# Optimization experiments

Hardware: AMD Instinct MI355X
Metric: run time of the kernel (lower is better)

Reference implementation:

```python
import jax, jax.numpy as jnp
from jax import lax
import numpy as np

COMMITMENT_COST = 0.25
N_EMBED = 512
EDIM = 32


def _conv(x, w, b, stride, pad):
    # x: NCHW, w: OIHW (torch Conv2d layout)
    y = lax.conv_general_dilated(x, w, (stride, stride), [(pad, pad), (pad, pad)],
                                 dimension_numbers=("NCHW", "OIHW", "NCHW"))
    return y + b[None, :, None, None]


def _conv_t(x, w, b, stride, pad):
    # torch ConvTranspose2d weight layout: (in, out, kH, kW)
    k = w.shape[2]
    w_ = jnp.flip(w, (2, 3)).transpose(1, 0, 2, 3)  # -> OIHW
    p = k - 1 - pad
    y = lax.conv_general_dilated(x, w_, (1, 1), [(p, p), (p, p)],
                                 lhs_dilation=(stride, stride),
                                 dimension_numbers=("NCHW", "OIHW", "NCHW"))
    return y + b[None, :, None, None]


def setup_inputs() -> dict:
    key = jax.random.key(0)
    ks = jax.random.split(key, 9)
    rn = lambda k, s: jax.random.normal(k, s, jnp.float32) * 0.05
    return {
        "x": jax.random.normal(ks[0], (32, 3, 256, 256), jnp.float32),
        "e_w1": rn(ks[1], (64, 3, 4, 4)),    "e_b1": jnp.zeros((64,), jnp.float32),
        "e_w2": rn(ks[2], (128, 64, 4, 4)),  "e_b2": jnp.zeros((128,), jnp.float32),
        "e_w3": rn(ks[3], (32, 128, 3, 3)),  "e_b3": jnp.zeros((32,), jnp.float32),
        "embed": jax.random.uniform(ks[4], (N_EMBED, EDIM), jnp.float32,
                                    -1.0 / N_EMBED, 1.0 / N_EMBED),
        "d_w1": rn(ks[5], (32, 128, 3, 3)),  "d_b1": jnp.zeros((128,), jnp.float32),
        "d_w2": rn(ks[6], (128, 64, 4, 4)),  "d_b2": jnp.zeros((64,), jnp.float32),
        "d_w3": rn(ks[7], (64, 3, 4, 4)),    "d_b3": jnp.zeros((3,), jnp.float32),
    }


def reference(x, e_w1, e_b1, e_w2, e_b2, e_w3, e_b3, embed,
              d_w1, d_b1, d_w2, d_b2, d_w3, d_b3):
    # ---- encoder ----
    h = jax.nn.relu(_conv(x, e_w1, e_b1, 2, 1))   # [B,64,128,128]
    h = jax.nn.relu(_conv(h, e_w2, e_b2, 2, 1))   # [B,128,64,64]
    z = jax.nn.relu(_conv(h, e_w3, e_b3, 1, 1))   # [B,32,64,64]
    # ---- vector quantizer ----
    zp = z.transpose(0, 2, 3, 1)                  # BHWC
    zf = zp.reshape(-1, EDIM)                     # [N, 32]
    d = (zf ** 2).sum(1, keepdims=True) + (embed ** 2).sum(1) \
        - 2.0 * zf @ embed.T                      # [N, n_embed]
    idx = jnp.argmin(d, axis=1)                   # [N]
    z_q = embed[idx].reshape(zp.shape)            # gather == onehot @ embed
    sg = lax.stop_gradient
    loss = jnp.mean((sg(z_q) - zp) ** 2) + COMMITMENT_COST * jnp.mean((z_q - sg(zp)) ** 2)
    z_q_st = zp + sg(z_q - zp)                    # straight-through
    z_q_st = z_q_st.transpose(0, 3, 1, 2)         # back to NCHW
    # ---- decoder ----
    h = jax.nn.relu(_conv_t(z_q_st, d_w1, d_b1, 1, 1))  # [B,128,64,64]
    h = jax.nn.relu(_conv_t(h, d_w2, d_b2, 2, 1))       # [B,64,128,128]
    x_recon = _conv_t(h, d_w3, d_b3, 2, 1)              # [B,3,256,256]
    return x_recon, loss
```

## Files before the change

### kernel.cpp

```cpp
#include <hip/hip_runtime.h>


typedef __attribute__((ext_vector_type(8))) short     short8;
typedef __attribute__((ext_vector_type(4))) short     s16x4;
typedef __attribute__((ext_vector_type(8))) __bf16    bf16x8;
typedef __attribute__((ext_vector_type(4))) float     f32x4;
typedef __attribute__((ext_vector_type(4))) unsigned  uint32x4;

__device__ __forceinline__ float b2f(unsigned short b) {
  union { unsigned u; float f; } v; v.u = ((unsigned)b) << 16; return v.f;
}
__device__ __forceinline__ unsigned short f2b(float f) {
  union { float f; unsigned u; } v; v.f = f;
  unsigned r = v.u + 0x7FFF + ((v.u >> 16) & 1);
  return (unsigned short)(r >> 16);
}

__global__ __launch_bounds__(256) void prepall_k(
    const float* __restrict__ ew1, const float* __restrict__ ew2,
    const float* __restrict__ ew3, const float* __restrict__ dw1,
    const float* __restrict__ dw2, const float* __restrict__ dw3,
    const float* __restrict__ emb,
    unsigned short* __restrict__ wq1, unsigned short* __restrict__ wq2,
    unsigned short* __restrict__ wq3, unsigned short* __restrict__ wq4,
    unsigned short* __restrict__ wq5, unsigned short* __restrict__ wq6,
    unsigned short* __restrict__ wqe, float* __restrict__ eng) {
  const int b = blockIdx.x;
  if (b < 64) {
    const int i = b*256 + threadIdx.x;
    const int j = i & 7, l = (i >> 3) & 63, ni = (i >> 9) & 3, nc = i >> 11;
    const int lm = l & 15, lk = l >> 4;
    wqe[i] = f2b(emb[(nc*64 + ni*16 + lm)*32 + lk*8 + j]);
    if (i < 512) {
      float s = 0.f;
      #pragma unroll
      for (int k = 0; k < 32; ++k) {
        const float f = b2f(f2b(emb[i*32 + k]));
        s = fmaf(f, f, s);
      }
      eng[i] = s;
    }
  } else if (b < 80) {
    const int i = (b - 64)*256 + threadIdx.x;
    const int j = i & 7, l = (i >> 3) & 63, ni = (i >> 9) & 3, ks = i >> 11;
    const int k = ks*32 + (l >> 4)*8 + j;
    const int co = ni*16 + (l & 15);
    wq1[i] = (k < 48) ? f2b(ew1[co*48 + k]) : (unsigned short)0;
  } else if (b < 592) {
    const int i = (b - 80)*256 + threadIdx.x;
    const int j = i & 7, l = (i >> 3) & 63, ni = (i >> 9) & 7, ks = i >> 12;
    const int lm = l & 15, lk = l >> 4;
    const int tap = ks >> 1, cc = ks & 1;
    const int co = ni*16 + lm, ci = cc*32 + lk*8 + j;
    wq2[i] = f2b(ew2[(co*64 + ci)*16 + tap]);
  } else if (b < 736) {
    const int i = (b - 592)*256 + threadIdx.x;
    const int j = i & 7, l = (i >> 3) & 63, ni = (i >> 9) & 1, ks = i >> 10;
    const int lm = l & 15, lk = l >> 4;
    const int tap = ks >> 2, cf = ks & 3;
    const int co = ni*16 + lm, ci = cf*32 + lk*8 + j;
    wq3[i] = f2b(ew3[(co*128 + ci)*9 + tap]);
  } else if (b < 880) {
    const int i = (b - 736)*256 + threadIdx.x;
    const int j = i & 7, l = (i >> 3) & 63, ni = (i >> 9) & 7, tap = i >> 12;
    const int lm = l & 15, lk = l >> 4;
    const int co = ni*16 + lm, ci = lk*8 + j;
    wq4[i] = f2b(dw1[(ci*128 + co)*9 + (8 - tap)]);
  } else if (b < 1392) {
    const int i = (b - 880)*256 + threadIdx.x;
    const int j = i & 7, l = (i >> 3) & 63, ni = (i >> 9) & 3;
    const int ks = (i >> 11) & 15, p = i >> 15;
    const int lm = l & 15, lk = l >> 4;
    const int py = p >> 1, px = p & 1;
    const int a = ks >> 3, bb = (ks >> 2) & 1, cc = ks & 3;
    const int co = ni*16 + lm, ci = cc*32 + lk*8 + j;
    const int ky = 3 - 2*a - py, kx = 3 - 2*bb - px;
    wq5[i] = f2b(dw2[(ci*64 + co)*16 + ky*4 + kx]);
  } else {
    const int i = (b - 1392)*256 + threadIdx.x;
    const int j = i & 7, l = (i >> 3) & 63, kc = (i >> 9) & 7, p = i >> 12;
    const int lm = l & 15, lk = l >> 4;
    const int a = kc >> 2, bb = (kc >> 1) & 1, ch = kc & 1;
    const int ci = ch*32 + lk*8 + j, co = lm;
    const int py = p >> 1, px = p & 1;
    const int ky = 2 - 2*a + (1 - py), kx = 2 - 2*bb + (1 - px);
    wq6[i] = (co < 3) ? f2b(dw3[(ci*3 + co)*16 + ky*4 + kx]) : (unsigned short)0;
  }
}

__global__ __launch_bounds__(256) void conv1m_k(const float* __restrict__ x,
    const unsigned short* __restrict__ wv, const float* __restrict__ bias,
    unsigned short* __restrict__ out) {
  __shared__ __align__(16) short RAW[12*264];
  __shared__ __align__(16) short IC[128*64];
  const int wid = ((blockIdx.x & 7) << 9) + (blockIdx.x >> 3);
  const int q = wid & 127, n = wid >> 7;
  for (int i = threadIdx.x; i < 396; i += 256)
    *(short8*)&RAW[i*8] = (short8)(short)0;
  __syncthreads();
  for (int s = threadIdx.x; s < 768; s += 256) {
    const int g = s >> 6, seg = s & 63;
    const int ci = g >> 2, ky = g & 3;
    const int iy = 2*q - 1 + ky;
    if (iy >= 0 && iy < 256) {
      const f32x4 v = *(const f32x4*)&x[((n*3 + ci)*256 + iy)*256 + seg*4];
      s16x4 sv;
      #pragma unroll
      for (int e = 0; e < 4; ++e) sv[e] = (short)f2b(v[e]);
      *(s16x4*)&RAW[g*264 + 4 + seg*4] = sv;
    }
  }
  __syncthreads();
  for (int s = threadIdx.x; s < 1024; s += 256) {
    const int kb = s & 7, ox = s >> 3;
    short8 v = (short8)(short)0;
    if (kb < 6) {
      const unsigned* u0 = (const unsigned*)&RAW[(2*kb  )*264 + 2*ox + 2];
      const unsigned* u1 = (const unsigned*)&RAW[(2*kb+1)*264 + 2*ox + 2];
      const unsigned a0 = u0[0], a1 = u0[1], a2 = u0[2];
      const unsigned b0 = u1[0], b1 = u1[1], b2 = u1[2];
      uint32x4 uv;
      uv[0] = (a0 >> 16) | (a1 << 16);
      uv[1] = (a1 >> 16) | (a2 << 16);
      uv[2] = (b0 >> 16) | (b1 << 16);
      uv[3] = (b1 >> 16) | (b2 << 16);
      v = __builtin_bit_cast(short8, uv);
    }
    const int bo = ((ox << 7) + (kb << 4)) ^ ((ox & 7) << 4);
    *(short8*)((char*)IC + bo) = v;
  }
  __syncthreads();
  const int w = threadIdx.x >> 6, l = threadIdx.x & 63;
  const int lm = l & 15, lk = l >> 4;
  f32x4 acc[2][4];
  #pragma unroll
  for (int mi = 0; mi < 2; ++mi)
    #pragma unroll
    for (int ni = 0; ni < 4; ++ni) acc[mi][ni] = (f32x4)0.0f;
  #pragma unroll
  for (int ks = 0; ks < 2; ++ks) {
    short8 bv[4];
    #pragma unroll
    for (int ni = 0; ni < 4; ++ni)
      bv[ni] = *(const short8*)(wv + (((ks*4 + ni)*64 + l) << 3));
    #pragma unroll
    for (int mi = 0; mi < 2; ++mi) {
      const int ox = w*32 + mi*16 + lm;
      const int bo = ((ox << 7) + (ks << 6) + (lk << 4)) ^ ((ox & 7) << 4);
      const short8 av = *(const short8*)((const char*)IC + bo);
      #pragma unroll
      for (int ni = 0; ni < 4; ++ni)
        acc[mi][ni] = __builtin_amdgcn_mfma_f32_16x16x32_bf16(
            __builtin_bit_cast(bf16x8, av),
            __builtin_bit_cast(bf16x8, bv[ni]),
            acc[mi][ni], 0, 0, 0);
    }
  }
  __syncthreads();
  #pragma unroll
  for (int mi = 0; mi < 2; ++mi)
    #pragma unroll
    for (int ni = 0; ni < 4; ++ni) {
      const int co = ni*16 + lm;
      const float bv = bias[co];
      #pragma unroll
      for (int r = 0; r < 4; ++r) {
        const int ox = w*32 + mi*16 + lk*4 + r;
        const int bo = ((ox << 7) + 2*co) ^ ((ox & 7) << 4);
        *(short*)((char*)IC + bo) = (short)f2b(fmaxf(acc[mi][ni][r] + bv, 0.f));
      }
    }
  __syncthreads();
  const long ob = ((long)(n*128 + q)) * 8192;
  for (int s = threadIdx.x; s < 1024; s += 256) {
    const int kb = s & 7, ox = s >> 3;
    const int bo = ((ox << 7) + (kb << 4)) ^ ((ox & 7) << 4);
    *(short8*)&out[ob + ox*64 + kb*8] = *(const short8*)((const char*)IC + bo);
  }
}

#define C2_LOAD(c) \
  _Pragma("unroll") \
  for (int s = 0; s < 9; ++s) { \
    st[s] = (short8)(short)0; \
    if (goff[s] >= 0) st[s] = *(const short8*)(in + goff[s] + (c)*32); \
  }
#define C2_WRITE \
  _Pragma("unroll") \
  for (int s = 0; s < 9; ++s) \
    if (lb[s] >= 0) *(short8*)((char*)IL + lb[s]) = st[s];
#define C2_COMPUTE(c) \
  _Pragma("unroll") \
  for (int t = 0; t < 16; ++t) { \
    const int ky = t >> 2, kx = t & 3; \
    const int p = 1 - (kx & 1), d = kx >> 1; \
    const short8 bv0 = *(const short8*)(wb + (t*2 + (c))*4096); \
    const short8 bv1 = *(const short8*)(wb + (t*2 + (c))*4096 + 512); \
    const char* Ab = (const char*)IL + (Bd0 + d*64); \
    const int imm0 = ((ky*2 + p)*66) << 6; \
    _Pragma("unroll") \
    for (int mi = 0; mi < 4; ++mi) { \
      const short8 av = *(const short8*)(Ab + imm0 + mi*1024); \
      acc[mi][0] = __builtin_amdgcn_mfma_f32_16x16x32_bf16( \
          __builtin_bit_cast(bf16x8, av), __builtin_bit_cast(bf16x8, bv0), \
          acc[mi][0], 0, 0, 0); \
      acc[mi][1] = __builtin_amdgcn_mfma_f32_16x16x32_bf16( \
          __builtin_bit_cast(bf16x8, av), __builtin_bit_cast(bf16x8, bv1), \
          acc[mi][1], 0, 0, 0); \
    } \
  }
__global__ __launch_bounds__(256) void conv2m_k(const unsigned short* __restrict__ in,
    const unsigned short* __restrict__ wv, const float* __restrict__ bias,
    unsigned short* __restrict__ out) {
  __shared__ short IL[8*66*32];
  const int wid = (blockIdx.x & 7)*256 + (blockIdx.x >> 3);
  const int q = wid & 63, n = wid >> 6;
  const int w = threadIdx.x >> 6, l = threadIdx.x & 63;
  const int lm = l & 15, lk = l >> 4;
  const int Bd0 = lm*64 + lk*16;
  const unsigned short* wb = wv + w*1024 + l*8;
  int goff[9], lb[9];
  #pragma unroll
  for (int s = 0; s < 9; ++s) {
    const int i = threadIdx.x + s*256;
    const int part = i & 3, e = i >> 2;
    const int idx = e % 66, rp = e / 66;
    const int r = rp >> 1, p = rp & 1;
    const int iy = 2*q - 1 + r, ix = 2*idx - p;
    const bool ok = (i < 2112) && iy >= 0 && iy < 128 && ix >= 0 && ix < 128;
    goff[s] = ok ? (((n*128 + iy)*128 + ix)*64 + part*8) : -1;
    lb[s]   = (i < 2112) ? (e*64 + part*16) : -1;
  }
  f32x4 acc[4][2];
  #pragma unroll
  for (int mi = 0; mi < 4; ++mi)
    #pragma unroll
    for (int ni = 0; ni < 2; ++ni) acc[mi][ni] = (f32x4)0.0f;
  short8 st[9];
  C2_LOAD(0); C2_WRITE;
  __syncthreads();
  C2_LOAD(1);
  C2_COMPUTE(0);
  __syncthreads();
  C2_WRITE;
  __syncthreads();
  C2_COMPUTE(1);
  __syncthreads();
  short* PB = (short*)IL;
  #pragma unroll
  for (int mi = 0; mi < 4; ++mi)
    #pragma unroll
    for (int r = 0; r < 4; ++r) {
      const int ox = mi*16 + lk*4 + r;
      #pragma unroll
      for (int ni = 0; ni < 2; ++ni) {
        const int co = (w*2 + ni)*16 + lm;
        PB[ox*144 + co] = (short)f2b(fmaxf(acc[mi][ni][r] + bias[co], 0.f));
      }
    }
  __syncthreads();
  {
    const int pos = threadIdx.x >> 2, coq = (threadIdx.x & 3) << 5;
    const long ob = ((long)((n*64 + q)*64 + pos))*128 + coq;
    #pragma unroll
    for (int u2 = 0; u2 < 4; ++u2)
      *(short8*)&out[ob + u2*8] = *(const short8*)&PB[pos*144 + coq + u2*8];
  }
}

#define C3_LOAD(c) \
  _Pragma("unroll") \
  for (int s = 0; s < 9; ++s) { \
    st[s] = (short8)(short)0; \
    if (goff[s] >= 0) st[s] = *(const short8*)(in + goff[s] + (c)*64); \
  }
#define C3_WRITE \
  _Pragma("unroll") \
  for (int s = 0; s < 9; ++s) \
    if (lb[s] >= 0) *(short8*)((char*)IL + lb[s]) = st[s];
#define C3_COMPUTE(c) \
  _Pragma("unroll") \
  for (int u = 0; u < 18; ++u) { \
    const int tap = u >> 1, cc = u & 1; \
    const int ky = tap / 3, kx = tap % 3; \
    const int ks = tap*4 + (c)*2 + cc; \
    const short8 bv0 = *(const short8*)(wb + ks*1024); \
    const short8 bv1 = *(const short8*)(wb + ks*1024 + 512); \
    const char* Ab = (const char*)IL + (Wc[kx][cc]); \
    const int imm0 = ky*8448; \
    _Pragma("unroll") \
    for (int mi = 0; mi < 2; ++mi) { \
      const short8 av = *(const short8*)(Ab + imm0 + mi*2048); \
      acc[mi][0] = __builtin_amdgcn_mfma_f32_16x16x32_bf16( \
          __builtin_bit_cast(bf16x8, av), __builtin_bit_cast(bf16x8, bv0), \
          acc[mi][0], 0, 0, 0); \
      acc[mi][1] = __builtin_amdgcn_mfma_f32_16x16x32_bf16( \
          __builtin_bit_cast(bf16x8, av), __builtin_bit_cast(bf16x8, bv1), \
          acc[mi][1], 0, 0, 0); \
    } \
  }
__global__ __launch_bounds__(256) void conv3v_k(const unsigned short* __restrict__ in,
    const unsigned short* __restrict__ wv, const float* __restrict__ bias,
    const unsigned short* __restrict__ wqe, const float* __restrict__ eng,
    const float* __restrict__ emb, float* __restrict__ zq,
    float* __restrict__ part) {
  __shared__ short IL[4*66*64];
  const int wid = (blockIdx.x & 7)*128 + (blockIdx.x >> 3);
  const int q = wid & 31, n = wid >> 5;
  const int w = threadIdx.x >> 6, l = threadIdx.x & 63;
  const int lm = l & 15, lk = l >> 4;
  const int row = w >> 1, oxb = (w & 1) * 32;
  int goff[9], lb[9];
  #pragma unroll
  for (int s = 0; s < 9; ++s) {
    const int i = threadIdx.x + s*256;
    const int part_ = i & 7, e = i >> 3;
    const int col = e % 66, r = e / 66;
    const int iy = 2*q - 1 + r, ix = col - 1;
    const bool ok = (i < 2112) && iy >= 0 && iy < 64 && ix >= 0 && ix < 64;
    goff[s] = ok ? (((n*64 + iy)*64 + ix)*128 + part_*8) : -1;
    lb[s]   = (i < 2112) ? ((e << 7) + ((part_ << 4) ^ ((col & 7) << 4))) : -1;
  }
  int Wc[3][2];
  #pragma unroll
  for (int kx = 0; kx < 3; ++kx) {
    const int e = oxb + lm + kx;
    Wc[kx][0] = row*8448 + (e << 7) + ((lk << 4) ^ ((e & 7) << 4));
    Wc[kx][1] = Wc[kx][0] ^ 0x40;
  }
  const unsigned short* wb = wv + l*8;
  f32x4 acc[2][2];
  #pragma unroll
  for (int mi = 0; mi < 2; ++mi)
    #pragma unroll
    for (int ni = 0; ni < 2; ++ni) acc[mi][ni] = (f32x4)0.0f;
  short8 st[9];
  C3_LOAD(0); C3_WRITE;
  __syncthreads();
  C3_LOAD(1);
  C3_COMPUTE(0);
  __syncthreads();
  C3_WRITE;
  __syncthreads();
  C3_COMPUTE(1);
  __syncthreads();
  short* ZB  = (short*)IL;
  float* ZF  = (float*)((char*)IL + 10240);
  int*  bidx = (int*)((char*)IL + 28672);
  float* red = (float*)((char*)IL + 29184);
  #pragma unroll
  for (int mi = 0; mi < 2; ++mi)
    #pragma unroll
    for (int ni = 0; ni < 2; ++ni) {
      const int co = ni*16 + lm;
      const float bv = bias[co];
      #pragma unroll
      for (int r = 0; r < 4; ++r) {
        const int pos = row*64 + oxb + mi*16 + lk*4 + r;
        const float v = fmaxf(acc[mi][ni][r] + bv, 0.f);
        ZB[pos*40 + co] = (short)f2b(v);
        ZF[pos*36 + co] = v;
      }
    }
  __syncthreads();
  short8 av[2];
  #pragma unroll
  for (int mi = 0; mi < 2; ++mi)
    av[mi] = *(const short8*)&ZB[(row*64 + oxb + mi*16 + lm)*40 + lk*8];
  float bd[2][4]; int bj[2][4];
  #pragma unroll
  for (int mi = 0; mi < 2; ++mi)
    #pragma unroll
    for (int r = 0; r < 4; ++r) { bd[mi][r] = 1e30f; bj[mi][r] = 0; }
  for (int nc = 0; nc < 8; ++nc) {
    f32x4 a2[2][4];
    #pragma unroll
    for (int mi = 0; mi < 2; ++mi)
      #pragma unroll
      for (int ni = 0; ni < 4; ++ni) a2[mi][ni] = (f32x4)0.0f;
    #pragma unroll
    for (int ni = 0; ni < 4; ++ni) {
      const short8 bv = *(const short8*)(wqe + (((nc*4 + ni)*64 + l) << 3));
      #pragma unroll
      for (int mi = 0; mi < 2; ++mi)
        a2[mi][ni] = __builtin_amdgcn_mfma_f32_16x16x32_bf16(
            __builtin_bit_cast(bf16x8, av[mi]),
            __builtin_bit_cast(bf16x8, bv),
            a2[mi][ni], 0, 0, 0);
    }
    #pragma unroll
    for (int ni = 0; ni < 4; ++ni) {
      const int j = nc*64 + ni*16 + lm;
      const float e_n = eng[j];
      #pragma unroll
      for (int mi = 0; mi < 2; ++mi)
        #pragma unroll
        for (int r = 0; r < 4; ++r) {
          const float d = fmaf(-2.f, a2[mi][ni][r], e_n);
          if (d < bd[mi][r]) { bd[mi][r] = d; bj[mi][r] = j; }
        }
    }
  }
  #pragma unroll
  for (int mi = 0; mi < 2; ++mi)
    #pragma unroll
    for (int r = 0; r < 4; ++r) {
      float d = bd[mi][r]; int j = bj[mi][r];
      #pragma unroll
      for (int off = 1; off < 16; off <<= 1) {
        const float od = __shfl_xor(d, off);
        const int   oj = __shfl_xor(j, off);
        if (od < d || (od == d && oj < j)) { d = od; j = oj; }
      }
      if (lm == 0) bidx[row*64 + oxb + mi*16 + lk*4 + r] = j;
    }
  __syncthreads();
  const int pl = threadIdx.x >> 1, hf = (threadIdx.x & 1) * 16;
  const int code = bidx[pl];
  const int oy2 = 2*q + (pl >> 6), ox2 = pl & 63;
  const long zqo = ((long)((n*64 + oy2)*64 + ox2)) * 32 + hf;
  float se = 0.f;
  #pragma unroll
  for (int qq = 0; qq < 4; ++qq) {
    const f32x4 ev = *(const f32x4*)&emb[code*32 + hf + qq*4];
    const f32x4 zv = *(const f32x4*)&ZF[pl*36 + hf + qq*4];
    *(f32x4*)&zq[zqo + qq*4] = ev;
    const f32x4 df = ev - zv;
    #pragma unroll
    for (int e = 0; e < 4; ++e) se = fmaf(df[e], df[e], se);
  }
  red[threadIdx.x] = se; __syncthreads();
  for (int s2 = 128; s2 > 0; s2 >>= 1) {
    if (threadIdx.x < s2) red[threadIdx.x] += red[threadIdx.x + s2];
    __syncthreads();
  }
  if (threadIdx.x == 0) part[blockIdx.x] = red[0];
}

__global__ __launch_bounds__(256) void d1m_k(const float* __restrict__ in,
    const unsigned short* __restrict__ wv, const float* __restrict__ bias,
    unsigned short* __restrict__ out) {
  __shared__ short IL[264*40];
  const int wid = (blockIdx.x & 7)*128 + (blockIdx.x >> 3);
  const int q = wid & 31, n = wid >> 5;
  const int w = threadIdx.x >> 6, l = threadIdx.x & 63;
  const int lm = l & 15, lk = l >> 4;
  const int row = w >> 1, oxb = (w & 1) * 32;
  for (int i = threadIdx.x; i < 1056; i += 256) {
    const int part = i & 3, e = i >> 2;
    const int col = e % 66, r = e / 66;
    const int iy = 2*q - 1 + r, ix = col - 1;
    short8 v = (short8)(short)0;
    if (iy >= 0 && iy < 64 && ix >= 0 && ix < 64) {
      const float* p = in + (((long)((n*64 + iy)*64 + ix)) * 32 + part*8);
      const f32x4 f0 = *(const f32x4*)p;
      const f32x4 f1 = *(const f32x4*)(p + 4);
      #pragma unroll
      for (int e2 = 0; e2 < 4; ++e2) {
        v[e2]     = (short)f2b(f0[e2]);
        v[e2 + 4] = (short)f2b(f1[e2]);
      }
    }
    *(short8*)&IL[e*40 + part*8] = v;
  }
  const unsigned short* wb = wv + l*8;
  int Wd[3];
  #pragma unroll
  for (int kx = 0; kx < 3; ++kx)
    Wd[kx] = row*5280 + (oxb + lm + kx)*80 + lk*16;
  __syncthreads();
  f32x4 acc[2][8];
  #pragma unroll
  for (int mi = 0; mi < 2; ++mi)
    #pragma unroll
    for (int ni = 0; ni < 8; ++ni) acc[mi][ni] = (f32x4)0.0f;
  #pragma unroll
  for (int tap = 0; tap < 9; ++tap) {
    const int ky = tap / 3, kx = tap % 3;
    short8 bv[8];
    #pragma unroll
    for (int ni = 0; ni < 8; ++ni)
      bv[ni] = *(const short8*)(wb + (tap*8 + ni)*512);
    const char* Ab = (const char*)IL + Wd[kx];
    const int imm0 = ky*5280;
    #pragma unroll
    for (int mi = 0; mi < 2; ++mi) {
      const short8 av = *(const short8*)(Ab + imm0 + mi*1280);
      #pragma unroll
      for (int ni = 0; ni < 8; ++ni)
        acc[mi][ni] = __builtin_amdgcn_mfma_f32_16x16x32_bf16(
            __builtin_bit_cast(bf16x8, av),
            __builtin_bit_cast(bf16x8, bv[ni]),
            acc[mi][ni], 0, 0, 0);
    }
  }
  short* PB = (short*)IL;
  #pragma unroll
  for (int rp = 0; rp < 2; ++rp) {
    __syncthreads();
    if (row == rp) {
      #pragma unroll
      for (int mi = 0; mi < 2; ++mi)
        #pragma unroll
        for (int r = 0; r < 4; ++r) {
          const int ox = oxb + mi*16 + lk*4 + r;
          #pragma unroll
          for (int ni = 0; ni < 8; ++ni) {
            const int co = ni*16 + lm;
            PB[ox*144 + co] = (short)f2b(fmaxf(acc[mi][ni][r] + bias[co], 0.f));
          }
        }
    }
    __syncthreads();
    const int pos = threadIdx.x >> 2, coq = (threadIdx.x & 3) << 5;
    const long ob = ((long)((n*64 + 2*q + rp)*64 + pos))*128 + coq;
    #pragma unroll
    for (int u2 = 0; u2 < 4; ++u2)
      *(short8*)&out[ob + u2*8] = *(const short8*)&PB[pos*144 + coq + u2*8];
  }
}

#define CT2_LOAD(c) \
  _Pragma("unroll") \
  for (int s = 0; s < 7; ++s) { \
    st[s] = (short8)(short)0; \
    if (goff[s] >= 0) st[s] = *(const short8*)(in + goff[s] + (c)*64); \
  }
#define CT2_WRITE \
  _Pragma("unroll") \
  for (int s = 0; s < 7; ++s) \
    if (lb[s] >= 0) *(short8*)((char*)IL + lb[s]) = st[s];
#define CT2_COMPUTE(c) \
  _Pragma("unroll") \
  for (int u = 0; u < 8; ++u) { \
    const int a = u >> 2, b = (u >> 1) & 1, c1 = u & 1; \
    const int ks = (a << 3) | (b << 2) | (2*(c) + c1); \
    short8 bv[4]; \
    _Pragma("unroll") \
    for (int ni = 0; ni < 4; ++ni) \
      bv[ni] = *(const short8*)(wb + ks*2048 + ni*512); \
    const char* Ab = (const char*)IL + (pyb + Wb[b][c1]); \
    const int imm0 = a*8448; \
    _Pragma("unroll") \
    for (int mi = 0; mi < 4; ++mi) { \
      const short8 av = *(const short8*)(Ab + imm0 + mi*2048); \
      _Pragma("unroll") \
      for (int ni = 0; ni < 4; ++ni) \
        acc[mi][ni] = __builtin_amdgcn_mfma_f32_16x16x32_bf16( \
            __builtin_bit_cast(bf16x8, av), \
            __builtin_bit_cast(bf16x8, bv[ni]), \
            acc[mi][ni], 0, 0, 0); \
    } \
  }
__global__ __launch_bounds__(256) void convt2m_k(const unsigned short* __restrict__ in,
    const unsigned short* __restrict__ wv, const float* __restrict__ bias,
    unsigned short* __restrict__ out) {
  __shared__ short IL[3*66*64];
  const int wid = (blockIdx.x & 7)*256 + (blockIdx.x >> 3);
  const int q = wid & 63, n = wid >> 6;
  const int w = threadIdx.x >> 6, l = threadIdx.x & 63;
  const int py = w >> 1, px = w & 1;
  const int lm = l & 15, lk = l >> 4;
  int Wb[2][2];
  #pragma unroll
  for (int b = 0; b < 2; ++b) {
    const int e = lm + px + b;
    Wb[b][0] = (e << 7) + ((lk << 4) ^ ((e & 7) << 4));
    Wb[b][1] = Wb[b][0] ^ 0x40;
  }
  const int pyb = py * 8448;
  const unsigned short* wb = wv + w*32768 + l*8;
  int goff[7], lb[7];
  #pragma unroll
  for (int s = 0; s < 7; ++s) {
    const int i = threadIdx.x + s*256;
    const int part = i & 7, e = i >> 3;
    const int col = e % 66, r = e / 66;
    const int iy = q - 1 + r, ix = col - 1;
    const bool ok = (i < 1584) && iy >= 0 && iy < 64 && ix >= 0 && ix < 64;
    goff[s] = ok ? (((n*64 + iy)*64 + ix)*128 + part*8) : -1;
    lb[s]   = (i < 1584) ? ((e << 7) + ((part << 4) ^ ((col & 7) << 4))) : -1;
  }
  f32x4 acc[4][4];
  #pragma unroll
  for (int mi = 0; mi < 4; ++mi)
    #pragma unroll
    for (int ni = 0; ni < 4; ++ni) acc[mi][ni] = (f32x4)0.0f;
  short8 st[7];
  CT2_LOAD(0); CT2_WRITE;
  __syncthreads();
  CT2_LOAD(1);
  CT2_COMPUTE(0);
  __syncthreads();
  CT2_WRITE;
  __syncthreads();
  CT2_COMPUTE(1);
  short* PB = (short*)IL;
  #pragma unroll
  for (int half = 0; half < 2; ++half) {
    __syncthreads();
    #pragma unroll
    for (int mi = 0; mi < 4; ++mi)
      #pragma unroll
      for (int r = 0; r < 4; ++r) {
        const int ox = 2*(mi*16 + lk*4 + r) + px;
        const int pos = py*128 + ox;
        #pragma unroll
        for (int nn = 0; nn < 2; ++nn) {
          const int co = (half*2 + nn)*16 + lm;
          PB[pos*40 + (co & 31)] =
              (short)f2b(fmaxf(acc[mi][half*2 + nn][r] + bias[co], 0.f));
        }
      }
    __syncthreads();
    const int pos = threadIdx.x;
    const long ob = ((long)((n*128 + 2*q + (pos >> 7))*128 + (pos & 127)))*64
                    + half*32;
    #pragma unroll
    for (int u2 = 0; u2 < 4; ++u2)
      *(short8*)&out[ob + u2*8] = *(const short8*)&PB[pos*40 + u2*8];
  }
}

__global__ __launch_bounds__(256) void loss_k(const float* __restrict__ part,
                                              float* __restrict__ out) {
  __shared__ float red[256];
  const int t = threadIdx.x;
  float s = 0.f;
  #pragma unroll
  for (int q = 0; q < 4; ++q) s += part[t + q*256];
  red[t] = s; __syncthreads();
  for (int st = 128; st > 0; st >>= 1) {
    if (t < st) red[t] += red[t + st];
    __syncthreads();
  }
  if (t == 0) out[0] = red[0] * (1.25f / (131072.f * 32.f));
}

__global__ __launch_bounds__(256) void convt3m_k(const unsigned short* __restrict__ in,
    const unsigned short* __restrict__ wq6, const float* __restrict__ bias,
    float* __restrict__ out) {
  __shared__ short8 IL[3*8*66];
  const int h = blockIdx.x & 1, q = (blockIdx.x >> 1) & 127, n = blockIdx.x >> 8;
  for (int i = threadIdx.x; i < 1584; i += 256) {
    const int c8 = i & 7, t = i >> 3, ixl = t % 66, r = t / 66;
    const int iy = q - 1 + r, ix = h*64 - 1 + ixl;
    short8 v = (short8)(short)0;
    if (iy >= 0 && iy < 128 && ix >= 0 && ix < 128)
      v = *(const short8*)(in + (((long)(n*128 + iy)*128 + ix)*64 + c8*8));
    IL[(r*8 + c8)*66 + ixl] = v;
  }
  const int w = threadIdx.x >> 6, l = threadIdx.x & 63;
  const int py = w >> 1, px = w & 1;
  const int lm = l & 15, lk = l >> 4;
  short8 bfrag[8];
  #pragma unroll
  for (int kc = 0; kc < 8; ++kc)
    bfrag[kc] = *(const short8*)(wq6 + (((w*8 + kc)*64 + l) << 3));
  __syncthreads();
  f32x4 acc[4];
  #pragma unroll
  for (int mi = 0; mi < 4; ++mi) acc[mi] = (f32x4)0.0f;
  #pragma unroll
  for (int kc = 0; kc < 8; ++kc) {
    const int a = kc >> 2, b = (kc >> 1) & 1, ch = kc & 1;
    const int base = (((py + a)*8 + ch*4 + lk)*66) + px + b;
    #pragma unroll
    for (int mi = 0; mi < 4; ++mi) {
      const short8 av = *(const short8*)&IL[base + mi*16 + lm];
      acc[mi] = __builtin_amdgcn_mfma_f32_16x16x32_bf16(
          __builtin_bit_cast(bf16x8, av),
          __builtin_bit_cast(bf16x8, bfrag[kc]),
          acc[mi], 0, 0, 0);
    }
  }
  __syncthreads();
  float* PB3 = (float*)IL;
  if (lm < 3) {
    const float bv = bias[lm];
    #pragma unroll
    for (int mi = 0; mi < 4; ++mi)
      #pragma unroll
      for (int r = 0; r < 4; ++r) {
        const int xq = mi*16 + lk*4 + r;
        PB3[(lm*2 + py)*128 + 2*xq + px] = acc[mi][r] + bv;
      }
  }
  __syncthreads();
  for (int t = threadIdx.x; t < 768; t += 256) {
    const int co = t >> 8, rem = t & 255, pyl = rem >> 7, xx = rem & 127;
    out[((long)(n*3 + co))*65536 + (2*q + pyl)*256 + h*128 + xx] = PB3[t];
  }
}

extern "C" void kernel_launch(void* const* d_in, const int* in_sizes, int n_in,
                              void* d_out, int out_size, void* d_ws, size_t ws_size,
                              hipStream_t stream) {
  const float* x   = (const float*)d_in[0];
  const float* ew1 = (const float*)d_in[1];  const float* eb1 = (const float*)d_in[2];
  const float* ew2 = (const float*)d_in[3];  const float* eb2 = (const float*)d_in[4];
  const float* ew3 = (const float*)d_in[5];  const float* eb3 = (const float*)d_in[6];
  const float* emb = (const float*)d_in[7];
  const float* dw1 = (const float*)d_in[8];  const float* db1 = (const float*)d_in[9];
  const float* dw2 = (const float*)d_in[10]; const float* db2 = (const float*)d_in[11];
  const float* dw3 = (const float*)d_in[12]; const float* db3 = (const float*)d_in[13];
  float* out = (float*)d_out;

  uint8_t* w8 = (uint8_t*)d_ws;
  unsigned short* h1 = (unsigned short*)w8;
  unsigned short* h2 = (unsigned short*)(w8 + 67108864);
  uint8_t* zr = w8 + 100663296;
  float* zq  = (float*)(w8 + 117440512);
  unsigned short* wqe = (unsigned short*)zr;
  float* eng = (float*)(zr + 32768);
  float* part = (float*)(zr + 36864);
  unsigned short* wq3 = (unsigned short*)(zr + 40960);
  unsigned short* wq4 = (unsigned short*)(zr + 131072);
  unsigned short* wq5 = (unsigned short*)(zr + 262144);
  unsigned short* wq6 = (unsigned short*)(zr + 524288);
  unsigned short* wq2 = (unsigned short*)(w8 + 117440512);
  unsigned short* wq1 = (unsigned short*)(w8 + 117440512 + 335872);
  unsigned short* d1 = h2;
  unsigned short* d2 = h1;

  prepall_k<<<dim3(1456),256,0,stream>>>(ew1, ew2, ew3, dw1, dw2, dw3, emb,
                                         wq1, wq2, wq3, wq4, wq5, wq6, wqe, eng);
  conv1m_k<<<dim3(4096),256,0,stream>>>(x, wq1, eb1, h1);
  conv2m_k<<<dim3(2048),256,0,stream>>>(h1, wq2, eb2, h2);
  conv3v_k<<<dim3(1024),256,0,stream>>>(h2, wq3, eb3, wqe, eng, emb, zq, part);
  loss_k<<<dim3(1),256,0,stream>>>(part, out + 6291456);
  d1m_k<<<dim3(1024),256,0,stream>>>(zq, wq4, db1, d1);
  convt2m_k<<<dim3(2048),256,0,stream>>>(d1, wq5, db2, d2);
  convt3m_k<<<dim3(8192),256,0,stream>>>(d2, wq6, db3, out);
}
```

Baseline: 340.5 us.

## Process two input rows per block in convt2m to share the halo row

The stride-2 transposed-conv kernel now has each 512-thread block handle two consecutive input rows (q0, q0+1) instead of one. The block loads a 4-row halo tile instead of two 3-row tiles, so the overlapping input rows are staged into LDS once and global loads for the halo drop. The grid is halved. The epilogue is serialized per row group, which adds extra barriers, and larger blocks with more LDS may lower occupancy.

Result: no change. 339.7 us (-0.2%).

```diff
diff --git a/kernel.cpp b/kernel.cpp
--- a/kernel.cpp
+++ b/kernel.cpp
@@ -522,13 +522,13 @@
 
 #define CT2_LOAD(c) \
   _Pragma("unroll") \
-  for (int s = 0; s < 7; ++s) { \
+  for (int s = 0; s < 5; ++s) { \
     st[s] = (short8)(short)0; \
     if (goff[s] >= 0) st[s] = *(const short8*)(in + goff[s] + (c)*64); \
   }
 #define CT2_WRITE \
   _Pragma("unroll") \
-  for (int s = 0; s < 7; ++s) \
+  for (int s = 0; s < 5; ++s) \
     if (lb[s] >= 0) *(short8*)((char*)IL + lb[s]) = st[s];
 #define CT2_COMPUTE(c) \
   _Pragma("unroll") \
@@ -552,14 +552,17 @@
             acc[mi][ni], 0, 0, 0); \
     } \
   }
-__global__ __launch_bounds__(256) void convt2m_k(const unsigned short* __restrict__ in,
+__global__ __launch_bounds__(512) void convt2m_k(const unsigned short* __restrict__ in,
     const unsigned short* __restrict__ wv, const float* __restrict__ bias,
     unsigned short* __restrict__ out) {
-  __shared__ short IL[3*66*64];
-  const int wid = (blockIdx.x & 7)*256 + (blockIdx.x >> 3);
-  const int q = wid & 63, n = wid >> 6;
-  const int w = threadIdx.x >> 6, l = threadIdx.x & 63;
-  const int py = w >> 1, px = w & 1;
+  __shared__ short IL[4*66*64];
+  const int wid = (blockIdx.x & 7)*128 + (blockIdx.x >> 3);
+  const int qp = wid & 31, n = wid >> 5;
+  const int q0 = 2*qp;
+  const int tid = threadIdx.x;
+  const int w = tid >> 6, l = tid & 63;
+  const int qi = w >> 2;
+  const int py = (w >> 1) & 1, px = w & 1;
   const int lm = l & 15, lk = l >> 4;
   int Wb[2][2];
   #pragma unroll
@@ -568,25 +571,25 @@
     Wb[b][0] = (e << 7) + ((lk << 4) ^ ((e & 7) << 4));
     Wb[b][1] = Wb[b][0] ^ 0x40;
   }
-  const int pyb = py * 8448;
-  const unsigned short* wb = wv + w*32768 + l*8;
-  int goff[7], lb[7];
-  #pragma unroll
-  for (int s = 0; s < 7; ++s) {
-    const int i = threadIdx.x + s*256;
+  const int pyb = (py + qi) * 8448;
+  const unsigned short* wb = wv + (w & 3)*32768 + l*8;
+  int goff[5], lb[5];
+  #pragma unroll
+  for (int s = 0; s < 5; ++s) {
+    const int i = tid + s*512;
     const int part = i & 7, e = i >> 3;
     const int col = e % 66, r = e / 66;
-    const int iy = q - 1 + r, ix = col - 1;
-    const bool ok = (i < 1584) && iy >= 0 && iy < 64 && ix >= 0 && ix < 64;
+    const int iy = q0 - 1 + r, ix = col - 1;
+    const bool ok = (i < 2112) && iy >= 0 && iy < 64 && ix >= 0 && ix < 64;
     goff[s] = ok ? (((n*64 + iy)*64 + ix)*128 + part*8) : -1;
-    lb[s]   = (i < 1584) ? ((e << 7) + ((part << 4) ^ ((col & 7) << 4))) : -1;
+    lb[s]   = (i < 2112) ? ((e << 7) + ((part << 4) ^ ((col & 7) << 4))) : -1;
   }
   f32x4 acc[4][4];
   #pragma unroll
   for (int mi = 0; mi < 4; ++mi)
     #pragma unroll
     for (int ni = 0; ni < 4; ++ni) acc[mi][ni] = (f32x4)0.0f;
-  short8 st[7];
+  short8 st[5];
   CT2_LOAD(0); CT2_WRITE;
   __syncthreads();
   CT2_LOAD(1);
@@ -597,29 +600,32 @@
   CT2_COMPUTE(1);
   short* PB = (short*)IL;
   #pragma unroll
-  for (int half = 0; half < 2; ++half) {
-    __syncthreads();
-    #pragma unroll
-    for (int mi = 0; mi < 4; ++mi)
-      #pragma unroll
-      for (int r = 0; r < 4; ++r) {
-        const int ox = 2*(mi*16 + lk*4 + r) + px;
-        const int pos = py*128 + ox;
+  for (int qq = 0; qq < 2; ++qq)
+    #pragma unroll
+    for (int half = 0; half < 2; ++half) {
+      __syncthreads();
+      if (qi == qq) {
         #pragma unroll
-        for (int nn = 0; nn < 2; ++nn) {
-          const int co = (half*2 + nn)*16 + lm;
-          PB[pos*40 + (co & 31)] =
-              (short)f2b(fmaxf(acc[mi][half*2 + nn][r] + bias[co], 0.f));
-        }
+        for (int mi = 0; mi < 4; ++mi)
+          #pragma unroll
+          for (int r = 0; r < 4; ++r) {
+            const int ox = 2*(mi*16 + lk*4 + r) + px;
+            const int pos = py*128 + ox;
+            #pragma unroll
+            for (int nn = 0; nn < 2; ++nn) {
+              const int co = (half*2 + nn)*16 + lm;
+              PB[pos*40 + (co & 31)] =
+                  (short)f2b(fmaxf(acc[mi][half*2 + nn][r] + bias[co], 0.f));
+            }
+          }
       }
-    __syncthreads();
-    const int pos = threadIdx.x;
-    const long ob = ((long)((n*128 + 2*q + (pos >> 7))*128 + (pos & 127)))*64
-                    + half*32;
-    #pragma unroll
-    for (int u2 = 0; u2 < 4; ++u2)
-      *(short8*)&out[ob + u2*8] = *(const short8*)&PB[pos*40 + u2*8];
-  }
+      __syncthreads();
+      const int pos = tid >> 1, hh = (tid & 1) << 4;
+      const long ob = ((long)((n*128 + 2*(q0 + qq) + (pos >> 7))*128
+                              + (pos & 127)))*64 + half*32 + hh;
+      *(short8*)&out[ob]     = *(const short8*)&PB[pos*40 + hh];
+      *(short8*)&out[ob + 8] = *(const short8*)&PB[pos*40 + hh + 8];
+    }
 }
 
 __global__ __launch_bounds__(256) void loss_k(const float* __restrict__ part,
@@ -730,6 +736,6 @@
   conv3v_k<<<dim3(1024),256,0,stream>>>(h2, wq3, eb3, wqe, eng, emb, zq, part);
   loss_k<<<dim3(1),256,0,stream>>>(part, out + 6291456);
   d1m_k<<<dim3(1024),256,0,stream>>>(zq, wq4, db1, d1);
-  convt2m_k<<<dim3(2048),256,0,stream>>>(d1, wq5, db2, d2);
+  convt2m_k<<<dim3(1024),512,0,stream>>>(d1, wq5, db2, d2);
   convt3m_k<<<dim3(8192),256,0,stream>>>(d2, wq6, db3, out);
 }
```
